# Kernel optimization log

Measured on AMD Instinct MI355X. Metric: run time of the kernel, lower is better.

Reference implementation:

```python
import jax, jax.numpy as jnp
import numpy as np

N_U, N_I, E = 100000, 100000, 600000
F_U, F_I, H, OUT = 96, 160, 128, 64
EPS = 1e-5


def _params(key):
    ks = jax.random.split(key, 20)
    n = lambda i, s: (jax.random.normal(ks[i], s, jnp.float32) * 0.05)
    p = {
        # lazy per-type input projections
        'Wp_u': n(0, (F_U, H)), 'bp_u': jnp.zeros((H,), jnp.float32),
        'Wp_i': n(1, (F_I, H)), 'bp_i': jnp.zeros((H,), jnp.float32),
        # layer 0 SAGE (in=H, out=H): lin_l (neighbors, bias), lin_r (root, no bias)
        'Wl0_ui': n(2, (H, H)), 'bl0_ui': jnp.zeros((H,), jnp.float32), 'Wr0_ui': n(3, (H, H)),
        'Wl0_iu': n(4, (H, H)), 'bl0_iu': jnp.zeros((H,), jnp.float32), 'Wr0_iu': n(5, (H, H)),
        'g0_u': jnp.ones((H,), jnp.float32), 'b0_u': jnp.zeros((H,), jnp.float32),
        'g0_i': jnp.ones((H,), jnp.float32), 'b0_i': jnp.zeros((H,), jnp.float32),
        # layer 1 SAGE (in=H, out=OUT)
        'Wl1_ui': n(6, (H, OUT)), 'bl1_ui': jnp.zeros((OUT,), jnp.float32), 'Wr1_ui': n(7, (H, OUT)),
        'Wl1_iu': n(8, (H, OUT)), 'bl1_iu': jnp.zeros((OUT,), jnp.float32), 'Wr1_iu': n(9, (H, OUT)),
        'g1_u': jnp.ones((OUT,), jnp.float32), 'b1_u': jnp.zeros((OUT,), jnp.float32),
        'g1_i': jnp.ones((OUT,), jnp.float32), 'b1_i': jnp.zeros((OUT,), jnp.float32),
    }
    return p


def setup_inputs() -> dict:
    key = jax.random.key(0)
    k0, k1, k2, k3, kp = jax.random.split(key, 5)
    inp = {
        'x_user': jax.random.normal(k0, (N_U, F_U), jnp.float32),
        'x_item': jax.random.normal(k1, (N_I, F_I), jnp.float32),
        'edge_ui': jax.random.randint(k2, (2, E), 0, N_U),  # row0: src user idx, row1: dst item idx
        'edge_iu': jax.random.randint(k3, (2, E), 0, N_I),  # row0: src item idx, row1: dst user idx
    }
    inp.update(_params(kp))
    return inp


def _seg_mean(x_src, src, dst, n_dst):
    # gather source features [E, C], scatter-mean into destinations [n_dst, C]
    msg = x_src[src]
    s = jax.ops.segment_sum(msg, dst, num_segments=n_dst)
    cnt = jax.ops.segment_sum(jnp.ones((dst.shape[0], 1), x_src.dtype), dst, num_segments=n_dst)
    return s / jnp.maximum(cnt, 1.0)


def _sage(x_src, x_dst, edge, Wl, bl, Wr, n_dst):
    agg = _seg_mean(x_src, edge[0], edge[1], n_dst)
    return agg @ Wl + bl + x_dst @ Wr


def _ln(h, g, b):
    m = jnp.mean(h, axis=-1, keepdims=True)
    v = jnp.mean(jnp.square(h - m), axis=-1, keepdims=True)
    return (h - m) * jax.lax.rsqrt(v + EPS) * g + b


def reference(x_user, x_item, edge_ui, edge_iu,
              Wp_u, bp_u, Wp_i, bp_i,
              Wl0_ui, bl0_ui, Wr0_ui, Wl0_iu, bl0_iu, Wr0_iu,
              g0_u, b0_u, g0_i, b0_i,
              Wl1_ui, bl1_ui, Wr1_ui, Wl1_iu, bl1_iu, Wr1_iu,
              g1_u, b1_u, g1_i, b1_i):
    # per-type input projection + ReLU
    h_u = jax.nn.relu(x_user @ Wp_u + bp_u)
    h_i = jax.nn.relu(x_item @ Wp_i + bp_i)
    # layer 0: HeteroConv(sum) of SAGEConv per edge type, then per-type LN + ReLU (dropout = eval identity)
    h_i1 = _sage(h_u, h_i, edge_ui, Wl0_ui, bl0_ui, Wr0_ui, N_I)
    h_u1 = _sage(h_i, h_u, edge_iu, Wl0_iu, bl0_iu, Wr0_iu, N_U)
    h_u1 = jax.nn.relu(_ln(h_u1, g0_u, b0_u))
    h_i1 = jax.nn.relu(_ln(h_i1, g0_i, b0_i))
    # layer 1 (final): SAGE -> LN, no ReLU/dropout
    h_i2 = _sage(h_u1, h_i1, edge_ui, Wl1_ui, bl1_ui, Wr1_ui, N_I)
    h_u2 = _sage(h_i1, h_u1, edge_iu, Wl1_iu, bl1_iu, Wr1_iu, N_U)
    h_u2 = _ln(h_u2, g1_u, b1_u)
    h_i2 = _ln(h_i2, g1_i, b1_i)
    return h_u2, h_i2
```

## Files before the change

kernel.cpp:

```cpp
#include <hip/hip_runtime.h>

typedef __attribute__((ext_vector_type(8))) __bf16 bf16x8;
typedef __attribute__((ext_vector_type(4))) float floatx4;
typedef __attribute__((ext_vector_type(8))) unsigned short ushort8v;
typedef __attribute__((ext_vector_type(4))) unsigned short ushort4v;

namespace {
constexpr int kNU = 100000, kNI = 100000, kE = 600000;
constexpr int kFU = 96, kFI = 160, kH = 128, kOUT = 64;
constexpr float kEPS = 1e-5f;
constexpr int kM = 32;
constexpr int kNCHUNK = 98;
constexpr int kNBLK = kNU / kM;
constexpr int kEB = (kE + 255) / 256;
constexpr int kPART = kNU / 8;
}

__device__ __forceinline__ unsigned short f2b(float f) {
  unsigned u = __builtin_bit_cast(unsigned, f);
  u += 0x7FFFu + ((u >> 16) & 1u);
  return (unsigned short)(u >> 16);
}
__device__ __forceinline__ float b2f(unsigned short h) {
  return __builtin_bit_cast(float, (unsigned)h << 16);
}
__device__ __forceinline__ void split3(float v, unsigned short& h,
                                       unsigned short& m, unsigned short& l) {
  h = f2b(v);
  const float r1 = v - b2f(h);
  m = f2b(r1);
  const float r2 = r1 - b2f(m);
  l = f2b(r2);
}
__device__ __forceinline__ void split2(float v, unsigned short& h,
                                       unsigned short& m) {
  h = f2b(v);
  m = f2b(v - b2f(h));
}
__device__ __forceinline__ bf16x8 ldb8(const unsigned short* p) {
  return __builtin_bit_cast(bf16x8, *(const ushort8v*)p);
}
__device__ __forceinline__ floatx4 mfma16(bf16x8 a, bf16x8 b, floatx4 c) {
  return __builtin_amdgcn_mfma_f32_16x16x32_bf16(a, b, c, 0, 0, 0);
}
__device__ __forceinline__ unsigned short* ab_ptr(void* base, int plane, int r,
                                                  int bo) {
  return (unsigned short*)((char*)base + plane * 8192 + r * 256 +
                           (bo ^ ((r & 7) << 4)));
}
__device__ __forceinline__ void gload_lds16(const void* g, void* l) {
  __builtin_amdgcn_global_load_lds(
      (const __attribute__((address_space(1))) void*)g,
      (__attribute__((address_space(3))) void*)l, 16, 0, 0);
}
__device__ __forceinline__ void split8(const float4& x, const float4& y,
                                       bf16x8& h8, bf16x8& m8) {
  ushort8v h, m;
  const float* p0 = &x.x;
  const float* p1 = &y.x;
#pragma unroll
  for (int u = 0; u < 4; ++u) {
    unsigned short th, tm;
    split2(p0[u], th, tm);
    h[u] = th; m[u] = tm;
    split2(p1[u], th, tm);
    h[4 + u] = th; m[4 + u] = tm;
  }
  h8 = __builtin_bit_cast(bf16x8, h);
  m8 = __builtin_bit_cast(bf16x8, m);
}

struct WcvtArgs {
  const float* src[10];
  unsigned short* dh[10];
  unsigned short* dm[10];
  unsigned short* dl[10];
  int K[10], N[10];
};
__global__ __launch_bounds__(256) void wcvt(WcvtArgs a) {
  const int m = blockIdx.y;
  const int K = a.K[m], N = a.N[m];
  const int idx = blockIdx.x * 256 + threadIdx.x;
  if (idx < K * N) {
    const int n = idx / K, k = idx - n * K;
    unsigned short h, mm, l;
    split3(a.src[m][(size_t)k * N + n], h, mm, l);
    a.dh[m][idx] = h;
    a.dm[m][idx] = mm;
    a.dl[m][idx] = l;
  }
}

__global__ void zero_int(int* __restrict__ p, int n) {
  int i = blockIdx.x * blockDim.x + threadIdx.x;
  const int st = gridDim.x * blockDim.x;
  for (; i < n; i += st) p[i] = 0;
}

__global__ __launch_bounds__(1024) void scanA(const int* __restrict__ cnt_u,
                                              const int* __restrict__ cnt_i,
                                              int* ptr_u, int* ptr_i, int* tot) {
  __shared__ int sh[1024];
  const int dir = blockIdx.y;
  const int* cnt = dir ? cnt_i : cnt_u;
  int* ptr = dir ? ptr_i : ptr_u;
  const int t = threadIdx.x;
  const int i = blockIdx.x * 1024 + t;
  const int v = (i < kNU) ? cnt[i] : 0;
  sh[t] = v;
  __syncthreads();
  for (int o = 1; o < 1024; o <<= 1) {
    const int y = (t >= o) ? sh[t - o] : 0;
    __syncthreads();
    sh[t] += y;
    __syncthreads();
  }
  if (i < kNU) ptr[i] = sh[t] - v;
  if (t == 1023) tot[dir * 128 + blockIdx.x] = sh[1023];
}

__global__ __launch_bounds__(128) void scanB(int* tot) {
  __shared__ int sh[128];
  int* tp = tot + blockIdx.x * 128;
  const int t = threadIdx.x;
  const int v = (t < kNCHUNK) ? tp[t] : 0;
  sh[t] = v;
  __syncthreads();
  for (int o = 1; o < 128; o <<= 1) {
    const int y = (t >= o) ? sh[t - o] : 0;
    __syncthreads();
    sh[t] += y;
    __syncthreads();
  }
  if (t < kNCHUNK) tp[t] = sh[t] - v;
}

__global__ __launch_bounds__(1024) void scanC(int* ptr_u, int* ptr_i,
                                              const int* __restrict__ tot,
                                              int* cur_u, int* cur_i) {
  const int dir = blockIdx.y;
  int* ptr = dir ? ptr_i : ptr_u;
  int* cur = dir ? cur_i : cur_u;
  const int i = blockIdx.x * 1024 + threadIdx.x;
  if (i < kNU) {
    const int v = ptr[i] + tot[dir * 128 + blockIdx.x];
    ptr[i] = v;
    cur[i] = v;
  }
}

template <int F>
__device__ __forceinline__ void proj_body(
    const float* __restrict__ x, const unsigned short* __restrict__ Wh,
    const unsigned short* __restrict__ Wm, const unsigned short* __restrict__ Wl,
    const float* __restrict__ bias, float* __restrict__ out, int blk,
    unsigned short* sh) {
  constexpr int AS = F + 8, KC = F / 32;
  unsigned short* Ah = sh;
  unsigned short* Am = sh + kM * AS;
  unsigned short* Al = sh + 2 * kM * AS;
  const int tid = threadIdx.x;
  const size_t row0 = (size_t)blk * kM;
  for (int c = tid; c < kM * (F / 4); c += 256) {
    const int r = c / (F / 4), j = c % (F / 4);
    const float4 v = *(const float4*)&x[(row0 + r) * F + j * 4];
    const float* vv = &v.x;
    ushort4v h4, m4, l4;
#pragma unroll
    for (int u = 0; u < 4; ++u) {
      unsigned short th, tm, tl;
      split3(vv[u], th, tm, tl);
      h4[u] = th; m4[u] = tm; l4[u] = tl;
    }
    *(ushort4v*)&Ah[r * AS + j * 4] = h4;
    *(ushort4v*)&Am[r * AS + j * 4] = m4;
    *(ushort4v*)&Al[r * AS + j * 4] = l4;
  }
  const int lane = tid & 63, w = tid >> 6, q = lane >> 4, ln = lane & 15;
  floatx4 acc[2][2] = {}, accL[2][2] = {};
  __syncthreads();
#pragma unroll
  for (int kc = 0; kc < KC; ++kc) {
    bf16x8 bh[2], bm[2], bl_[2];
#pragma unroll
    for (int t = 0; t < 2; ++t) {
      const int off = (w * 32 + t * 16 + ln) * F + kc * 32 + q * 8;
      bh[t] = ldb8(&Wh[off]);
      bm[t] = ldb8(&Wm[off]);
      bl_[t] = ldb8(&Wl[off]);
    }
#pragma unroll
    for (int mt = 0; mt < 2; ++mt) {
      const int ro = mt * 16 + ln, co = kc * 32 + q * 8;
      const bf16x8 ah = ldb8(&Ah[ro * AS + co]);
      const bf16x8 am = ldb8(&Am[ro * AS + co]);
      const bf16x8 al = ldb8(&Al[ro * AS + co]);
#pragma unroll
      for (int t = 0; t < 2; ++t) {
        acc[mt][t] = mfma16(ah, bh[t], acc[mt][t]);
        floatx4 cl = accL[mt][t];
        cl = mfma16(ah, bm[t], cl);
        cl = mfma16(am, bh[t], cl);
        cl = mfma16(ah, bl_[t], cl);
        cl = mfma16(al, bh[t], cl);
        cl = mfma16(am, bm[t], cl);
        accL[mt][t] = cl;
      }
    }
  }
#pragma unroll
  for (int t = 0; t < 2; ++t) {
    const int col = w * 32 + t * 16 + ln;
    const float bv = bias[col];
#pragma unroll
    for (int mt = 0; mt < 2; ++mt)
#pragma unroll
      for (int r = 0; r < 4; ++r)
        out[(row0 + mt * 16 + q * 4 + r) * kH + col] =
            fmaxf((acc[mt][t][r] + accL[mt][t][r]) + bv, 0.f);
  }
}

__global__ __launch_bounds__(256, 4) void hist_proj(
    const int* __restrict__ eui, const int* __restrict__ eiu, int* cnt_i,
    int* cnt_u, const float* __restrict__ x,
    const unsigned short* __restrict__ Wh, const unsigned short* __restrict__ Wm,
    const unsigned short* __restrict__ Wl, const float* __restrict__ bias,
    float* __restrict__ out) {
  __shared__ __align__(16) unsigned short sh[3 * kM * (kFU + 8)];
  if (blockIdx.x < 8 * kEB) {
    const int part = blockIdx.x & 7, slice = blockIdx.x >> 3;
    const int e = slice * 256 + threadIdx.x;
    if (e < kE) {
      const int di = eui[kE + e];
      if (di / kPART == part) atomicAdd(&cnt_i[di], 1);
      const int du = eiu[kE + e];
      if (du / kPART == part) atomicAdd(&cnt_u[du], 1);
    }
  } else {
    proj_body<kFU>(x, Wh, Wm, Wl, bias, out, blockIdx.x - 8 * kEB, sh);
  }
}

__global__ __launch_bounds__(256, 4) void fill_proj(
    const int* __restrict__ eui, const int* __restrict__ eiu, int* cur_i,
    int* cur_u, int* __restrict__ col_ui, int* __restrict__ col_iu,
    const float* __restrict__ x, const unsigned short* __restrict__ Wh,
    const unsigned short* __restrict__ Wm, const unsigned short* __restrict__ Wl,
    const float* __restrict__ bias, float* __restrict__ out) {
  __shared__ __align__(16) unsigned short sh[3 * kM * (kFI + 8)];
  if (blockIdx.x < 8 * kEB) {
    const int part = blockIdx.x & 7, slice = blockIdx.x >> 3;
    const int e = slice * 256 + threadIdx.x;
    if (e < kE) {
      const int di = eui[kE + e];
      if (di / kPART == part) {
        const int p = atomicAdd(&cur_i[di], 1);
        col_ui[p] = eui[e];
      }
      const int du = eiu[kE + e];
      if (du / kPART == part) {
        const int p2 = atomicAdd(&cur_u[du], 1);
        col_iu[p2] = eiu[e];
      }
    }
  } else {
    proj_body<kFI>(x, Wh, Wm, Wl, bias, out, blockIdx.x - 8 * kEB, sh);
  }
}

struct AggArgs {
  const float* src[2];
  const int* ptr[2];
  const int* cur[2];
  const int* col[2];
  float* out[2];
};
template <int W>
__global__ __launch_bounds__(256) void agg2(AggArgs a) {
  const int dir = blockIdx.y;
  const int w = threadIdx.x >> 6, lane = threadIdx.x & 63;
  const int row = blockIdx.x * 4 + w;
  const float* __restrict__ feat = a.src[dir];
  const int* __restrict__ col = a.col[dir];
  const int beg = a.ptr[dir][row], end = a.cur[dir][row];
  const float inv = 1.0f / fmaxf((float)(end - beg), 1.0f);
  if (W == 128) {
    float s0 = 0.f, s1 = 0.f;
    for (int e = beg; e < end; e += 8) {
      const int n = end - e;
      int cidx[8];
#pragma unroll
      for (int j = 0; j < 8; ++j) cidx[j] = col[(j < n) ? (e + j) : e];
      __builtin_amdgcn_sched_barrier(0);
      float2 v[8];
#pragma unroll
      for (int j = 0; j < 8; ++j)
        if (j < n) v[j] = *(const float2*)&feat[(size_t)cidx[j] * 128 + lane * 2];
      __builtin_amdgcn_sched_barrier(0);
#pragma unroll
      for (int j = 0; j < 8; ++j)
        if (j < n) { s0 += v[j].x; s1 += v[j].y; }
    }
    float2 o;
    o.x = s0 * inv;
    o.y = s1 * inv;
    *(float2*)&a.out[dir][(size_t)row * 128 + lane * 2] = o;
  } else {
    float s = 0.f;
    for (int e = beg; e < end; e += 8) {
      const int n = end - e;
      int cidx[8];
#pragma unroll
      for (int j = 0; j < 8; ++j) cidx[j] = col[(j < n) ? (e + j) : e];
      __builtin_amdgcn_sched_barrier(0);
      float v[8];
#pragma unroll
      for (int j = 0; j < 8; ++j)
        if (j < n) v[j] = feat[(size_t)cidx[j] * 64 + lane];
      __builtin_amdgcn_sched_barrier(0);
#pragma unroll
      for (int j = 0; j < 8; ++j)
        if (j < n) s += v[j];
    }
    a.out[dir][(size_t)row * 64 + lane] = s * inv;
  }
}

struct FsArgs {
  const float* agg[2];
  const float* root[2];
  const unsigned short *WLh[2], *WLm[2];
  const unsigned short *WRh[2], *WRm[2];
  const unsigned short *ZBh[2], *ZBm[2];
  const float *bl[2], *g[2], *b[2];
  float* out[2];
  float* zout[2];
};
__global__ __launch_bounds__(256, 4) void sage0(FsArgs a) {
  constexpr int NOUT = 128;
  __shared__ __align__(16) char Lds[32768];
  float* Cs = (float*)Lds;
  const int tid = threadIdx.x;
  const int dir = blockIdx.y;
  const size_t row0 = (size_t)blockIdx.x * kM;
  const float* __restrict__ agg = a.agg[dir];
  const float* __restrict__ root = a.root[dir];
  const unsigned short* __restrict__ WLh = a.WLh[dir];
  const unsigned short* __restrict__ WLm = a.WLm[dir];
  const unsigned short* __restrict__ WRh = a.WRh[dir];
  const unsigned short* __restrict__ WRm = a.WRm[dir];
  const int lane = tid & 63, w = tid >> 6, q = lane >> 4, ln = lane & 15;

  {
    const char* g0 = (const char*)agg + row0 * 512;
    const char* g1 = (const char*)root + row0 * 512;
#pragma unroll
    for (int c = 0; c < 4; ++c) {
      const int sbase = (w * 4 + c) * 1024;
      const int s = sbase + lane * 16;
      const int soff = s ^ (((s >> 9) & 7) << 4);
      gload_lds16(g0 + soff, Lds + sbase);
      gload_lds16(g1 + soff, Lds + 16384 + sbase);
    }
  }

  floatx4 acc[2][2] = {}, accL[2][2] = {};
  __syncthreads();
#pragma unroll
  for (int kc = 0; kc < 4; ++kc) {
    bf16x8 BL[2][2], BR[2][2];
#pragma unroll
    for (int t = 0; t < 2; ++t) {
      const int off = (w * 32 + t * 16 + ln) * kH + kc * 32 + q * 8;
      BL[0][t] = ldb8(&WLh[off]);
      BL[1][t] = ldb8(&WLm[off]);
      BR[0][t] = ldb8(&WRh[off]);
      BR[1][t] = ldb8(&WRm[off]);
    }
#pragma unroll
    for (int mt = 0; mt < 2; ++mt) {
      const int ro = mt * 16 + ln;
      const int lb = ro * 512 + kc * 128 + q * 32;
      const int xr = (ro & 7) << 4;
      const float4 fa0 = *(const float4*)(Lds + (lb ^ xr));
      const float4 fa1 = *(const float4*)(Lds + ((lb + 16) ^ xr));
      const float4 fr0 = *(const float4*)(Lds + 16384 + (lb ^ xr));
      const float4 fr1 = *(const float4*)(Lds + 16384 + ((lb + 16) ^ xr));
      bf16x8 a1h, a1m, a2h, a2m;
      split8(fa0, fa1, a1h, a1m);
      split8(fr0, fr1, a2h, a2m);
#pragma unroll
      for (int t = 0; t < 2; ++t) {
        floatx4 c = acc[mt][t];
        c = mfma16(a1h, BL[0][t], c);
        c = mfma16(a2h, BR[0][t], c);
        acc[mt][t] = c;
        floatx4 cl = accL[mt][t];
        cl = mfma16(a1h, BL[1][t], cl);
        cl = mfma16(a1m, BL[0][t], cl);
        cl = mfma16(a2h, BR[1][t], cl);
        cl = mfma16(a2m, BR[0][t], cl);
        accL[mt][t] = cl;
      }
    }
  }
  __syncthreads();
  const float* __restrict__ blv = a.bl[dir];
#pragma unroll
  for (int t = 0; t < 2; ++t) {
    const int colx = (w * 2 + t) * 16 + ln;
    const float bv = blv[colx];
#pragma unroll
    for (int mt = 0; mt < 2; ++mt)
#pragma unroll
      for (int r = 0; r < 4; ++r)
        Cs[(mt * 16 + q * 4 + r) * (NOUT + 1) + colx] =
            (acc[mt][t][r] + accL[mt][t][r]) + bv;
  }
  __syncthreads();
  const int r = tid >> 3, sub = tid & 7;
  const float* __restrict__ gg = a.g[dir];
  const float* __restrict__ bb = a.b[dir];
  float vals[16], s = 0.f;
#pragma unroll
  for (int j = 0; j < 16; ++j) {
    const float v = Cs[r * (NOUT + 1) + sub * 16 + j];
    vals[j] = v;
    s += v;
  }
#pragma unroll
  for (int o = 1; o < 8; o <<= 1) s += __shfl_xor(s, o, 64);
  const float mean = s * (1.0f / NOUT);
  float s2 = 0.f;
#pragma unroll
  for (int j = 0; j < 16; ++j) {
    const float d = vals[j] - mean;
    s2 += d * d;
  }
#pragma unroll
  for (int o = 1; o < 8; o <<= 1) s2 += __shfl_xor(s2, o, 64);
  const float rstd = rsqrtf(s2 * (1.0f / NOUT) + kEPS);
  float* op = a.out[dir] + (row0 + r) * NOUT + sub * 16;
  float zv[16];
#pragma unroll
  for (int j = 0; j < 16; j += 4) {
    float4 o4;
    float* oo = &o4.x;
#pragma unroll
    for (int jj = 0; jj < 4; ++jj) {
      const float hv = fmaxf((vals[j + jj] - mean) * rstd * gg[sub * 16 + j + jj] +
                                 bb[sub * 16 + j + jj],
                             0.f);
      oo[jj] = hv;
      zv[j + jj] = hv;
    }
    *(float4*)&op[j] = o4;
  }
  __syncthreads();
#pragma unroll
  for (int j = 0; j < 16; j += 8) {
    ushort8v h8, m8;
#pragma unroll
    for (int u = 0; u < 8; ++u) {
      unsigned short th, tm;
      split2(zv[j + u], th, tm);
      h8[u] = th; m8[u] = tm;
    }
    const int bo = sub * 32 + j * 2;
    *(ushort8v*)ab_ptr(Lds, 0, r, bo) = h8;
    *(ushort8v*)ab_ptr(Lds, 1, r, bo) = m8;
  }
  const unsigned short* __restrict__ ZBh = a.ZBh[dir];
  const unsigned short* __restrict__ ZBm = a.ZBm[dir];
  floatx4 zacc[2] = {}, zaccL[2] = {};
  __syncthreads();
#pragma unroll
  for (int kc = 0; kc < 4; ++kc) {
    const int off = (w * 16 + ln) * kH + kc * 32 + q * 8;
    const bf16x8 zbh = ldb8(&ZBh[off]);
    const bf16x8 zbm = ldb8(&ZBm[off]);
#pragma unroll
    for (int mt = 0; mt < 2; ++mt) {
      const int ro = mt * 16 + ln, cob = kc * 64 + q * 16;
      const bf16x8 ah = ldb8(ab_ptr(Lds, 0, ro, cob));
      const bf16x8 am = ldb8(ab_ptr(Lds, 1, ro, cob));
      zacc[mt] = mfma16(ah, zbh, zacc[mt]);
      floatx4 cl = zaccL[mt];
      cl = mfma16(ah, zbm, cl);
      cl = mfma16(am, zbh, cl);
      zaccL[mt] = cl;
    }
  }
  float* __restrict__ zo = a.zout[dir];
  const int zcol = w * 16 + ln;
#pragma unroll
  for (int mt = 0; mt < 2; ++mt)
#pragma unroll
    for (int rr = 0; rr < 4; ++rr)
      zo[(row0 + mt * 16 + q * 4 + rr) * kOUT + zcol] =
          zacc[mt][rr] + zaccL[mt][rr];
}

struct S1Args {
  const float* root[2];
  const float* aggz[2];
  const unsigned short *Bh[2], *Bm[2];
  const float *bl[2], *g[2], *b[2];
  float* out[2];
};
__global__ __launch_bounds__(256, 5) void sage1(S1Args a) {
  constexpr int NOUT = kOUT;
  __shared__ __align__(16) unsigned short Ab[2 * kM * kH];
  float* Cs = (float*)Ab;
  const int tid = threadIdx.x, dir = blockIdx.y;
  const size_t row0 = (size_t)blockIdx.x * kM;
  const float* __restrict__ root = a.root[dir];
  const unsigned short* __restrict__ Bh = a.Bh[dir];
  const unsigned short* __restrict__ Bm = a.Bm[dir];
  const int lane = tid & 63, w = tid >> 6, q = lane >> 4, ln = lane & 15;

  float4 va[4];
#pragma unroll
  for (int k = 0; k < 4; ++k) {
    const int c = tid + k * 256, r = c >> 5, j = c & 31;
    va[k] = *(const float4*)&root[(row0 + r) * kH + j * 4];
  }
  bf16x8 Bh4[4], Bm4[4];
#pragma unroll
  for (int kc = 0; kc < 4; ++kc) {
    const int off = (w * 16 + ln) * kH + kc * 32 + q * 8;
    Bh4[kc] = ldb8(&Bh[off]);
    Bm4[kc] = ldb8(&Bm[off]);
  }
  __builtin_amdgcn_sched_barrier(0);
#pragma unroll
  for (int k = 0; k < 4; ++k) {
    const int c = tid + k * 256, r = c >> 5, j = c & 31;
    const float* vv = &va[k].x;
    ushort4v h4, m4;
#pragma unroll
    for (int u = 0; u < 4; ++u) {
      unsigned short th, tm;
      split2(vv[u], th, tm);
      h4[u] = th; m4[u] = tm;
    }
    *(ushort4v*)ab_ptr(Ab, 0, r, j * 8) = h4;
    *(ushort4v*)ab_ptr(Ab, 1, r, j * 8) = m4;
  }
  floatx4 acc[2] = {}, accL[2] = {};
  __syncthreads();
#pragma unroll
  for (int kc = 0; kc < 4; ++kc) {
#pragma unroll
    for (int mt = 0; mt < 2; ++mt) {
      const int ro = mt * 16 + ln, cob = kc * 64 + q * 16;
      const bf16x8 ah = ldb8(ab_ptr(Ab, 0, ro, cob));
      const bf16x8 am = ldb8(ab_ptr(Ab, 1, ro, cob));
      acc[mt] = mfma16(ah, Bh4[kc], acc[mt]);
      floatx4 cl = accL[mt];
      cl = mfma16(ah, Bm4[kc], cl);
      cl = mfma16(am, Bh4[kc], cl);
      accL[mt] = cl;
    }
  }
  __syncthreads();
  const float* __restrict__ blv = a.bl[dir];
  {
    const int col = w * 16 + ln;
    const float bv = blv[col];
#pragma unroll
    for (int mt = 0; mt < 2; ++mt)
#pragma unroll
      for (int r = 0; r < 4; ++r)
        Cs[(mt * 16 + q * 4 + r) * (NOUT + 1) + col] =
            (acc[mt][r] + accL[mt][r]) + bv;
  }
  __syncthreads();
  const int r = tid >> 3, sub = tid & 7;
  const float* __restrict__ az = a.aggz[dir];
  const float* __restrict__ gg = a.g[dir];
  const float* __restrict__ bb = a.b[dir];
  const float4 az0 = *(const float4*)&az[(row0 + r) * NOUT + sub * 8];
  const float4 az1 = *(const float4*)&az[(row0 + r) * NOUT + sub * 8 + 4];
  float vals[8], s = 0.f;
#pragma unroll
  for (int j = 0; j < 8; ++j) {
    const float v = Cs[r * (NOUT + 1) + sub * 8 + j] +
                    (j < 4 ? (&az0.x)[j] : (&az1.x)[j - 4]);
    vals[j] = v;
    s += v;
  }
#pragma unroll
  for (int o = 1; o < 8; o <<= 1) s += __shfl_xor(s, o, 64);
  const float mean = s * (1.0f / NOUT);
  float s2 = 0.f;
#pragma unroll
  for (int j = 0; j < 8; ++j) {
    const float d = vals[j] - mean;
    s2 += d * d;
  }
#pragma unroll
  for (int o = 1; o < 8; o <<= 1) s2 += __shfl_xor(s2, o, 64);
  const float rstd = rsqrtf(s2 * (1.0f / NOUT) + kEPS);
  float* op = a.out[dir] + (row0 + r) * NOUT + sub * 8;
#pragma unroll
  for (int j = 0; j < 8; j += 4) {
    float4 o4;
    float* oo = &o4.x;
#pragma unroll
    for (int jj = 0; jj < 4; ++jj)
      oo[jj] = (vals[j + jj] - mean) * rstd * gg[sub * 8 + j + jj] +
               bb[sub * 8 + j + jj];
    *(float4*)&op[j] = o4;
  }
}

extern "C" void kernel_launch(void* const* d_in, const int* in_sizes, int n_in,
                              void* d_out, int out_size, void* d_ws, size_t ws_size,
                              hipStream_t stream) {
  (void)in_sizes; (void)n_in; (void)out_size; (void)ws_size;
  const float* x_u    = (const float*)d_in[0];
  const float* x_i    = (const float*)d_in[1];
  const int*   e_ui   = (const int*)d_in[2];
  const int*   e_iu   = (const int*)d_in[3];
  const float* Wp_u   = (const float*)d_in[4];
  const float* bp_u   = (const float*)d_in[5];
  const float* Wp_i   = (const float*)d_in[6];
  const float* bp_i   = (const float*)d_in[7];
  const float* Wl0_ui = (const float*)d_in[8];
  const float* bl0_ui = (const float*)d_in[9];
  const float* Wr0_ui = (const float*)d_in[10];
  const float* Wl0_iu = (const float*)d_in[11];
  const float* bl0_iu = (const float*)d_in[12];
  const float* Wr0_iu = (const float*)d_in[13];
  const float* g0_u   = (const float*)d_in[14];
  const float* b0_u   = (const float*)d_in[15];
  const float* g0_i   = (const float*)d_in[16];
  const float* b0_i   = (const float*)d_in[17];
  const float* Wl1_ui = (const float*)d_in[18];
  const float* bl1_ui = (const float*)d_in[19];
  const float* Wr1_ui = (const float*)d_in[20];
  const float* Wl1_iu = (const float*)d_in[21];
  const float* bl1_iu = (const float*)d_in[22];
  const float* Wr1_iu = (const float*)d_in[23];
  const float* g1_u   = (const float*)d_in[24];
  const float* b1_u   = (const float*)d_in[25];
  const float* g1_i   = (const float*)d_in[26];
  const float* b1_i   = (const float*)d_in[27];

  float* pf = (float*)d_ws;
  const size_t NH = (size_t)kNU * kH;
  float* hu0 = pf;
  float* hi0 = pf + NH;
  float* b2  = pf + 2 * NH;
  float* b3  = pf + 3 * NH;
  float* aggzI = hi0;
  float* aggzU = hi0 + (size_t)kNU * kOUT;
  unsigned short* wh = (unsigned short*)(pf + 4 * NH);
  unsigned short* wm = wh + 131072;
  unsigned short* wl = wm + 131072;
  int* pi = (int*)(wl + 131072);
  int* cnt_u = pi; pi += kNU;
  int* cnt_i = pi; pi += kNU;
  int* ptr_u = pi; pi += kNU;
  int* ptr_i = pi; pi += kNU;
  int* cur_u = pi; pi += kNU;
  int* cur_i = pi; pi += kNU;
  int* tot   = pi; pi += 2 * 128;
  int* col_ui = pi; pi += kE;
  int* col_iu = pi; pi += kE;

  const int oPu = 0, oPi = 12288, o0Lui = 32768, o0Rui = 49152,
            o0Liu = 65536, o0Riu = 81920, o1Lui = 98304, o1Rui = 106496,
            o1Liu = 114688, o1Riu = 122880;

  float* out_u = (float*)d_out;
  float* out_i = out_u + (size_t)kNU * kOUT;
  float* Zu = out_u;
  float* Zi = out_i;

  WcvtArgs wa;
  const float* wsrc[10] = {Wp_u, Wp_i, Wl0_ui, Wr0_ui, Wl0_iu, Wr0_iu,
                           Wl1_ui, Wr1_ui, Wl1_iu, Wr1_iu};
  const int woff[10] = {oPu, oPi, o0Lui, o0Rui, o0Liu, o0Riu,
                        o1Lui, o1Rui, o1Liu, o1Riu};
  const int wK[10] = {kFU, kFI, kH, kH, kH, kH, kH, kH, kH, kH};
  const int wN[10] = {kH, kH, kH, kH, kH, kH, kOUT, kOUT, kOUT, kOUT};
  for (int i = 0; i < 10; ++i) {
    wa.src[i] = wsrc[i];
    wa.dh[i] = wh + woff[i];
    wa.dm[i] = wm + woff[i];
    wa.dl[i] = wl + woff[i];
    wa.K[i] = wK[i];
    wa.N[i] = wN[i];
  }
  wcvt<<<dim3(80, 10), 256, 0, stream>>>(wa);

  zero_int<<<256, 256, 0, stream>>>(cnt_u, 2 * kNU);
  hist_proj<<<8 * kEB + kNBLK, 256, 0, stream>>>(e_ui, e_iu, cnt_i, cnt_u, x_u,
                                                 wh + oPu, wm + oPu, wl + oPu,
                                                 bp_u, hu0);
  scanA<<<dim3(kNCHUNK, 2), 1024, 0, stream>>>(cnt_u, cnt_i, ptr_u, ptr_i, tot);
  scanB<<<2, 128, 0, stream>>>(tot);
  scanC<<<dim3(kNCHUNK, 2), 1024, 0, stream>>>(ptr_u, ptr_i, tot, cur_u, cur_i);
  fill_proj<<<8 * kEB + kNBLK, 256, 0, stream>>>(e_ui, e_iu, cur_i, cur_u,
                                                 col_ui, col_iu, x_i, wh + oPi,
                                                 wm + oPi, wl + oPi, bp_i, hi0);

  AggArgs g0;
  g0.src[0] = hu0; g0.ptr[0] = ptr_i; g0.cur[0] = cur_i; g0.col[0] = col_ui;
  g0.out[0] = b2;
  g0.src[1] = hi0; g0.ptr[1] = ptr_u; g0.cur[1] = cur_u; g0.col[1] = col_iu;
  g0.out[1] = b3;
  agg2<kH><<<dim3(kNU / 4, 2), 256, 0, stream>>>(g0);

  FsArgs a0;
  a0.agg[0] = b2; a0.root[0] = hi0;
  a0.WLh[0] = wh + o0Lui; a0.WLm[0] = wm + o0Lui;
  a0.WRh[0] = wh + o0Rui; a0.WRm[0] = wm + o0Rui;
  a0.ZBh[0] = wh + o1Liu; a0.ZBm[0] = wm + o1Liu;
  a0.bl[0] = bl0_ui; a0.g[0] = g0_i; a0.b[0] = b0_i;
  a0.out[0] = b2;
  a0.zout[0] = Zi;
  a0.agg[1] = b3; a0.root[1] = hu0;
  a0.WLh[1] = wh + o0Liu; a0.WLm[1] = wm + o0Liu;
  a0.WRh[1] = wh + o0Riu; a0.WRm[1] = wm + o0Riu;
  a0.ZBh[1] = wh + o1Lui; a0.ZBm[1] = wm + o1Lui;
  a0.bl[1] = bl0_iu; a0.g[1] = g0_u; a0.b[1] = b0_u;
  a0.out[1] = b3;
  a0.zout[1] = Zu;
  sage0<<<dim3(kNBLK, 2), 256, 0, stream>>>(a0);

  AggArgs g1;
  g1.src[0] = Zu; g1.ptr[0] = ptr_i; g1.cur[0] = cur_i; g1.col[0] = col_ui;
  g1.out[0] = aggzI;
  g1.src[1] = Zi; g1.ptr[1] = ptr_u; g1.cur[1] = cur_u; g1.col[1] = col_iu;
  g1.out[1] = aggzU;
  agg2<kOUT><<<dim3(kNU / 4, 2), 256, 0, stream>>>(g1);

  S1Args s1;
  s1.root[0] = b2; s1.aggz[0] = aggzI;
  s1.Bh[0] = wh + o1Rui; s1.Bm[0] = wm + o1Rui;
  s1.bl[0] = bl1_ui; s1.g[0] = g1_i; s1.b[0] = b1_i; s1.out[0] = out_i;
  s1.root[1] = b3; s1.aggz[1] = aggzU;
  s1.Bh[1] = wh + o1Riu; s1.Bm[1] = wm + o1Riu;
  s1.bl[1] = bl1_iu; s1.g[1] = g1_u; s1.b[1] = b1_u; s1.out[1] = out_u;
  sage1<<<dim3(kNBLK, 2), 256, 0, stream>>>(s1);
}
```

Measured before the change: 713.3 us.

## Store intermediate features as pre-split swizzled bf16 hi/lo planes

```diff
diff --git a/kernel.cpp b/kernel.cpp
--- a/kernel.cpp
+++ b/kernel.cpp
@@ -37,7 +37,7 @@
   h = f2b(v);
   m = f2b(v - b2f(h));
 }
-__device__ __forceinline__ bf16x8 ldb8(const unsigned short* p) {
+__device__ __forceinline__ bf16x8 ldb8(const void* p) {
   return __builtin_bit_cast(bf16x8, *(const ushort8v*)p);
 }
 __device__ __forceinline__ floatx4 mfma16(bf16x8 a, bf16x8 b, floatx4 c) {
@@ -53,22 +53,7 @@
       (const __attribute__((address_space(1))) void*)g,
       (__attribute__((address_space(3))) void*)l, 16, 0, 0);
 }
-__device__ __forceinline__ void split8(const float4& x, const float4& y,
-                                       bf16x8& h8, bf16x8& m8) {
-  ushort8v h, m;
-  const float* p0 = &x.x;
-  const float* p1 = &y.x;
-#pragma unroll
-  for (int u = 0; u < 4; ++u) {
-    unsigned short th, tm;
-    split2(p0[u], th, tm);
-    h[u] = th; m[u] = tm;
-    split2(p1[u], th, tm);
-    h[4 + u] = th; m[4 + u] = tm;
-  }
-  h8 = __builtin_bit_cast(bf16x8, h);
-  m8 = __builtin_bit_cast(bf16x8, m);
-}
+
 
 struct WcvtArgs {
   const float* src[10];
@@ -153,7 +138,7 @@
 __device__ __forceinline__ void proj_body(
     const float* __restrict__ x, const unsigned short* __restrict__ Wh,
     const unsigned short* __restrict__ Wm, const unsigned short* __restrict__ Wl,
-    const float* __restrict__ bias, float* __restrict__ out, int blk,
+    const float* __restrict__ bias, unsigned short* __restrict__ out, int blk,
     unsigned short* sh) {
   constexpr int AS = F + 8, KC = F / 32;
   unsigned short* Ah = sh;
@@ -215,9 +200,16 @@
 #pragma unroll
     for (int mt = 0; mt < 2; ++mt)
 #pragma unroll
-      for (int r = 0; r < 4; ++r)
-        out[(row0 + mt * 16 + q * 4 + r) * kH + col] =
-            fmaxf((acc[mt][t][r] + accL[mt][t][r]) + bv, 0.f);
+      for (int r = 0; r < 4; ++r) {
+        const int rl = mt * 16 + q * 4 + r;
+        const float val = fmaxf((acc[mt][t][r] + accL[mt][t][r]) + bv, 0.f);
+        unsigned short hh, mm;
+        split2(val, hh, mm);
+        char* rowp = (char*)out + (row0 + rl) * 512;
+        const int bo = (col * 2) ^ ((rl & 7) << 4);
+        *(unsigned short*)(rowp + bo) = hh;
+        *(unsigned short*)(rowp + 256 + bo) = mm;
+      }
   }
 }
 
@@ -226,7 +218,7 @@
     int* cnt_u, const float* __restrict__ x,
     const unsigned short* __restrict__ Wh, const unsigned short* __restrict__ Wm,
     const unsigned short* __restrict__ Wl, const float* __restrict__ bias,
-    float* __restrict__ out) {
+    unsigned short* __restrict__ out) {
   __shared__ __align__(16) unsigned short sh[3 * kM * (kFU + 8)];
   if (blockIdx.x < 8 * kEB) {
     const int part = blockIdx.x & 7, slice = blockIdx.x >> 3;
@@ -247,7 +239,7 @@
     int* cur_u, int* __restrict__ col_ui, int* __restrict__ col_iu,
     const float* __restrict__ x, const unsigned short* __restrict__ Wh,
     const unsigned short* __restrict__ Wm, const unsigned short* __restrict__ Wl,
-    const float* __restrict__ bias, float* __restrict__ out) {
+    const float* __restrict__ bias, unsigned short* __restrict__ out) {
   __shared__ __align__(16) unsigned short sh[3 * kM * (kFI + 8)];
   if (blockIdx.x < 8 * kEB) {
     const int part = blockIdx.x & 7, slice = blockIdx.x >> 3;
@@ -270,22 +262,22 @@
 }
 
 struct AggArgs {
-  const float* src[2];
+  const void* src[2];
   const int* ptr[2];
   const int* cur[2];
   const int* col[2];
-  float* out[2];
+  void* out[2];
 };
 template <int W>
 __global__ __launch_bounds__(256) void agg2(AggArgs a) {
   const int dir = blockIdx.y;
   const int w = threadIdx.x >> 6, lane = threadIdx.x & 63;
   const int row = blockIdx.x * 4 + w;
-  const float* __restrict__ feat = a.src[dir];
   const int* __restrict__ col = a.col[dir];
   const int beg = a.ptr[dir][row], end = a.cur[dir][row];
   const float inv = 1.0f / fmaxf((float)(end - beg), 1.0f);
   if (W == 128) {
+    const char* __restrict__ Tb = (const char*)a.src[dir];
     float s0 = 0.f, s1 = 0.f;
     for (int e = beg; e < end; e += 8) {
       const int n = end - e;
@@ -293,20 +285,35 @@
 #pragma unroll
       for (int j = 0; j < 8; ++j) cidx[j] = col[(j < n) ? (e + j) : e];
       __builtin_amdgcn_sched_barrier(0);
-      float2 v[8];
+      unsigned hm0[8], hm1[8];
 #pragma unroll
       for (int j = 0; j < 8; ++j)
-        if (j < n) v[j] = *(const float2*)&feat[(size_t)cidx[j] * 128 + lane * 2];
+        if (j < n) {
+          const char* rp = Tb + (size_t)cidx[j] * 512;
+          const int bo = (lane * 4) ^ ((cidx[j] & 7) << 4);
+          hm0[j] = *(const unsigned*)(rp + bo);
+          hm1[j] = *(const unsigned*)(rp + 256 + bo);
+        }
       __builtin_amdgcn_sched_barrier(0);
 #pragma unroll
       for (int j = 0; j < 8; ++j)
-        if (j < n) { s0 += v[j].x; s1 += v[j].y; }
-    }
-    float2 o;
-    o.x = s0 * inv;
-    o.y = s1 * inv;
-    *(float2*)&a.out[dir][(size_t)row * 128 + lane * 2] = o;
+        if (j < n) {
+          s0 += b2f((unsigned short)hm0[j]) + b2f((unsigned short)hm1[j]);
+          s1 += b2f((unsigned short)(hm0[j] >> 16)) +
+                b2f((unsigned short)(hm1[j] >> 16));
+        }
+    }
+    s0 *= inv;
+    s1 *= inv;
+    unsigned short h0, m0, h1, m1;
+    split2(s0, h0, m0);
+    split2(s1, h1, m1);
+    char* op = (char*)a.out[dir] + (size_t)row * 512;
+    const int bo = (lane * 4) ^ ((row & 7) << 4);
+    *(unsigned*)(op + bo) = (unsigned)h0 | ((unsigned)h1 << 16);
+    *(unsigned*)(op + 256 + bo) = (unsigned)m0 | ((unsigned)m1 << 16);
   } else {
+    const float* __restrict__ feat = (const float*)a.src[dir];
     float s = 0.f;
     for (int e = beg; e < end; e += 8) {
       const int n = end - e;
@@ -323,29 +330,38 @@
       for (int j = 0; j < 8; ++j)
         if (j < n) s += v[j];
     }
-    a.out[dir][(size_t)row * 64 + lane] = s * inv;
+    ((float*)a.out[dir])[(size_t)row * 64 + lane] = s * inv;
   }
 }
 
 struct FsArgs {
-  const float* agg[2];
-  const float* root[2];
+  const unsigned short* agg[2];
+  const unsigned short* root[2];
   const unsigned short *WLh[2], *WLm[2];
   const unsigned short *WRh[2], *WRm[2];
   const unsigned short *ZBh[2], *ZBm[2];
   const float *bl[2], *g[2], *b[2];
-  float* out[2];
+  unsigned short* out[2];
   float* zout[2];
 };
-__global__ __launch_bounds__(256, 4) void sage0(FsArgs a) {
+
+#define LOADW_S0(B, KC)                                                  \
+  {                                                                      \
+    const int o0_ = (w * 32 + 0 * 16 + ln) * kH + (KC) * 32 + q * 8;     \
+    const int o1_ = (w * 32 + 1 * 16 + ln) * kH + (KC) * 32 + q * 8;     \
+    BLh[B][0] = ldb8(&WLh[o0_]); BLh[B][1] = ldb8(&WLh[o1_]);            \
+    BLm[B][0] = ldb8(&WLm[o0_]); BLm[B][1] = ldb8(&WLm[o1_]);            \
+    BRh[B][0] = ldb8(&WRh[o0_]); BRh[B][1] = ldb8(&WRh[o1_]);            \
+    BRm[B][0] = ldb8(&WRm[o0_]); BRm[B][1] = ldb8(&WRm[o1_]);            \
+  }
+
+__global__ __launch_bounds__(256, 5) void sage0(FsArgs a) {
   constexpr int NOUT = 128;
   __shared__ __align__(16) char Lds[32768];
   float* Cs = (float*)Lds;
   const int tid = threadIdx.x;
   const int dir = blockIdx.y;
   const size_t row0 = (size_t)blockIdx.x * kM;
-  const float* __restrict__ agg = a.agg[dir];
-  const float* __restrict__ root = a.root[dir];
   const unsigned short* __restrict__ WLh = a.WLh[dir];
   const unsigned short* __restrict__ WLm = a.WLm[dir];
   const unsigned short* __restrict__ WRh = a.WRh[dir];
@@ -353,54 +369,45 @@
   const int lane = tid & 63, w = tid >> 6, q = lane >> 4, ln = lane & 15;
 
   {
-    const char* g0 = (const char*)agg + row0 * 512;
-    const char* g1 = (const char*)root + row0 * 512;
+    const char* g0 = (const char*)a.agg[dir] + row0 * 512;
+    const char* g1 = (const char*)a.root[dir] + row0 * 512;
 #pragma unroll
     for (int c = 0; c < 4; ++c) {
       const int sbase = (w * 4 + c) * 1024;
-      const int s = sbase + lane * 16;
-      const int soff = s ^ (((s >> 9) & 7) << 4);
-      gload_lds16(g0 + soff, Lds + sbase);
-      gload_lds16(g1 + soff, Lds + 16384 + sbase);
-    }
-  }
-
+      gload_lds16(g0 + sbase + lane * 16, Lds + sbase);
+      gload_lds16(g1 + sbase + lane * 16, Lds + 16384 + sbase);
+    }
+  }
+  bf16x8 BLh[2][2], BLm[2][2], BRh[2][2], BRm[2][2];
+  LOADW_S0(0, 0);
   floatx4 acc[2][2] = {}, accL[2][2] = {};
   __syncthreads();
 #pragma unroll
   for (int kc = 0; kc < 4; ++kc) {
-    bf16x8 BL[2][2], BR[2][2];
-#pragma unroll
-    for (int t = 0; t < 2; ++t) {
-      const int off = (w * 32 + t * 16 + ln) * kH + kc * 32 + q * 8;
-      BL[0][t] = ldb8(&WLh[off]);
-      BL[1][t] = ldb8(&WLm[off]);
-      BR[0][t] = ldb8(&WRh[off]);
-      BR[1][t] = ldb8(&WRm[off]);
-    }
+    if (kc < 3) LOADW_S0((kc + 1) & 1, kc + 1);
+    __builtin_amdgcn_sched_barrier(0);
 #pragma unroll
     for (int mt = 0; mt < 2; ++mt) {
       const int ro = mt * 16 + ln;
-      const int lb = ro * 512 + kc * 128 + q * 32;
       const int xr = (ro & 7) << 4;
-      const float4 fa0 = *(const float4*)(Lds + (lb ^ xr));
-      const float4 fa1 = *(const float4*)(Lds + ((lb + 16) ^ xr));
-      const float4 fr0 = *(const float4*)(Lds + 16384 + (lb ^ xr));
-      const float4 fr1 = *(const float4*)(Lds + 16384 + ((lb + 16) ^ xr));
-      bf16x8 a1h, a1m, a2h, a2m;
-      split8(fa0, fa1, a1h, a1m);
-      split8(fr0, fr1, a2h, a2m);
+      const int hb = (kc * 64 + q * 16) ^ xr;
+      const char* r1 = Lds + ro * 512;
+      const char* r2 = Lds + 16384 + ro * 512;
+      const bf16x8 a1h = ldb8(r1 + hb);
+      const bf16x8 a1m = ldb8(r1 + 256 + hb);
+      const bf16x8 a2h = ldb8(r2 + hb);
+      const bf16x8 a2m = ldb8(r2 + 256 + hb);
 #pragma unroll
       for (int t = 0; t < 2; ++t) {
         floatx4 c = acc[mt][t];
-        c = mfma16(a1h, BL[0][t], c);
-        c = mfma16(a2h, BR[0][t], c);
+        c = mfma16(a1h, BLh[kc & 1][t], c);
+        c = mfma16(a2h, BRh[kc & 1][t], c);
         acc[mt][t] = c;
         floatx4 cl = accL[mt][t];
-        cl = mfma16(a1h, BL[1][t], cl);
-        cl = mfma16(a1m, BL[0][t], cl);
-        cl = mfma16(a2h, BR[1][t], cl);
-        cl = mfma16(a2m, BR[0][t], cl);
+        cl = mfma16(a1h, BLm[kc & 1][t], cl);
+        cl = mfma16(a1m, BLh[kc & 1][t], cl);
+        cl = mfma16(a2h, BRm[kc & 1][t], cl);
+        cl = mfma16(a2m, BRh[kc & 1][t], cl);
         accL[mt][t] = cl;
       }
     }
@@ -441,36 +448,38 @@
 #pragma unroll
   for (int o = 1; o < 8; o <<= 1) s2 += __shfl_xor(s2, o, 64);
   const float rstd = rsqrtf(s2 * (1.0f / NOUT) + kEPS);
-  float* op = a.out[dir] + (row0 + r) * NOUT + sub * 16;
   float zv[16];
-#pragma unroll
-  for (int j = 0; j < 16; j += 4) {
-    float4 o4;
-    float* oo = &o4.x;
-#pragma unroll
-    for (int jj = 0; jj < 4; ++jj) {
-      const float hv = fmaxf((vals[j + jj] - mean) * rstd * gg[sub * 16 + j + jj] +
-                                 bb[sub * 16 + j + jj],
-                             0.f);
-      oo[jj] = hv;
-      zv[j + jj] = hv;
-    }
-    *(float4*)&op[j] = o4;
-  }
-  __syncthreads();
-#pragma unroll
-  for (int j = 0; j < 16; j += 8) {
-    ushort8v h8, m8;
-#pragma unroll
-    for (int u = 0; u < 8; ++u) {
+  ushort8v h8[2], m8[2];
+#pragma unroll
+  for (int hf = 0; hf < 2; ++hf)
+#pragma unroll
+    for (int j = 0; j < 8; ++j) {
+      const int jj = hf * 8 + j;
+      const float hv = fmaxf(
+          (vals[jj] - mean) * rstd * gg[sub * 16 + jj] + bb[sub * 16 + jj], 0.f);
+      zv[jj] = hv;
       unsigned short th, tm;
-      split2(zv[j + u], th, tm);
-      h8[u] = th; m8[u] = tm;
-    }
-    const int bo = sub * 32 + j * 2;
-    *(ushort8v*)ab_ptr(Lds, 0, r, bo) = h8;
-    *(ushort8v*)ab_ptr(Lds, 1, r, bo) = m8;
-  }
+      split2(hv, th, tm);
+      h8[hf][j] = th;
+      m8[hf][j] = tm;
+    }
+  {
+    char* hp = (char*)a.out[dir] + (row0 + r) * 512;
+    const int xr = (r & 7) << 4;
+#pragma unroll
+    for (int hf = 0; hf < 2; ++hf) {
+      const int bo = (sub * 32 + hf * 16) ^ xr;
+      *(ushort8v*)(hp + bo) = h8[hf];
+      *(ushort8v*)(hp + 256 + bo) = m8[hf];
+    }
+  }
+  __syncthreads();
+#pragma unroll
+  for (int hf = 0; hf < 2; ++hf) {
+    *(ushort8v*)ab_ptr(Lds, 0, r, sub * 32 + hf * 16) = h8[hf];
+    *(ushort8v*)ab_ptr(Lds, 1, r, sub * 32 + hf * 16) = m8[hf];
+  }
+  (void)zv;
   const unsigned short* __restrict__ ZBh = a.ZBh[dir];
   const unsigned short* __restrict__ ZBm = a.ZBm[dir];
   floatx4 zacc[2] = {}, zaccL[2] = {};
@@ -503,28 +512,29 @@
 }
 
 struct S1Args {
-  const float* root[2];
+  const unsigned short* root[2];
   const float* aggz[2];
   const unsigned short *Bh[2], *Bm[2];
   const float *bl[2], *g[2], *b[2];
   float* out[2];
 };
-__global__ __launch_bounds__(256, 5) void sage1(S1Args a) {
+__global__ __launch_bounds__(256, 6) void sage1(S1Args a) {
   constexpr int NOUT = kOUT;
-  __shared__ __align__(16) unsigned short Ab[2 * kM * kH];
-  float* Cs = (float*)Ab;
+  __shared__ __align__(16) char Lds[16384];
+  float* Cs = (float*)Lds;
   const int tid = threadIdx.x, dir = blockIdx.y;
   const size_t row0 = (size_t)blockIdx.x * kM;
-  const float* __restrict__ root = a.root[dir];
   const unsigned short* __restrict__ Bh = a.Bh[dir];
   const unsigned short* __restrict__ Bm = a.Bm[dir];
   const int lane = tid & 63, w = tid >> 6, q = lane >> 4, ln = lane & 15;
 
-  float4 va[4];
-#pragma unroll
-  for (int k = 0; k < 4; ++k) {
-    const int c = tid + k * 256, r = c >> 5, j = c & 31;
-    va[k] = *(const float4*)&root[(row0 + r) * kH + j * 4];
+  {
+    const char* g0 = (const char*)a.root[dir] + row0 * 512;
+#pragma unroll
+    for (int c = 0; c < 4; ++c) {
+      const int sbase = (w * 4 + c) * 1024;
+      gload_lds16(g0 + sbase + lane * 16, Lds + sbase);
+    }
   }
   bf16x8 Bh4[4], Bm4[4];
 #pragma unroll
@@ -533,30 +543,18 @@
     Bh4[kc] = ldb8(&Bh[off]);
     Bm4[kc] = ldb8(&Bm[off]);
   }
-  __builtin_amdgcn_sched_barrier(0);
-#pragma unroll
-  for (int k = 0; k < 4; ++k) {
-    const int c = tid + k * 256, r = c >> 5, j = c & 31;
-    const float* vv = &va[k].x;
-    ushort4v h4, m4;
-#pragma unroll
-    for (int u = 0; u < 4; ++u) {
-      unsigned short th, tm;
-      split2(vv[u], th, tm);
-      h4[u] = th; m4[u] = tm;
-    }
-    *(ushort4v*)ab_ptr(Ab, 0, r, j * 8) = h4;
-    *(ushort4v*)ab_ptr(Ab, 1, r, j * 8) = m4;
-  }
   floatx4 acc[2] = {}, accL[2] = {};
   __syncthreads();
 #pragma unroll
   for (int kc = 0; kc < 4; ++kc) {
 #pragma unroll
     for (int mt = 0; mt < 2; ++mt) {
-      const int ro = mt * 16 + ln, cob = kc * 64 + q * 16;
-      const bf16x8 ah = ldb8(ab_ptr(Ab, 0, ro, cob));
-      const bf16x8 am = ldb8(ab_ptr(Ab, 1, ro, cob));
+      const int ro = mt * 16 + ln;
+      const int xr = (ro & 7) << 4;
+      const int hb = (kc * 64 + q * 16) ^ xr;
+      const char* rp = Lds + ro * 512;
+      const bf16x8 ah = ldb8(rp + hb);
+      const bf16x8 am = ldb8(rp + 256 + hb);
       acc[mt] = mfma16(ah, Bh4[kc], acc[mt]);
       floatx4 cl = accL[mt];
       cl = mfma16(ah, Bm4[kc], cl);
@@ -651,12 +649,12 @@
 
   float* pf = (float*)d_ws;
   const size_t NH = (size_t)kNU * kH;
-  float* hu0 = pf;
-  float* hi0 = pf + NH;
-  float* b2  = pf + 2 * NH;
-  float* b3  = pf + 3 * NH;
-  float* aggzI = hi0;
-  float* aggzU = hi0 + (size_t)kNU * kOUT;
+  unsigned short* Thu0 = (unsigned short*)pf;
+  unsigned short* Thi0 = (unsigned short*)(pf + NH);
+  unsigned short* TaggI = (unsigned short*)(pf + 2 * NH);
+  unsigned short* TaggU = (unsigned short*)(pf + 3 * NH);
+  float* aggzI = pf + NH;
+  float* aggzU = pf + NH + (size_t)kNU * kOUT;
   unsigned short* wh = (unsigned short*)(pf + 4 * NH);
   unsigned short* wm = wh + 131072;
   unsigned short* wl = wm + 131072;
@@ -700,35 +698,35 @@
   zero_int<<<256, 256, 0, stream>>>(cnt_u, 2 * kNU);
   hist_proj<<<8 * kEB + kNBLK, 256, 0, stream>>>(e_ui, e_iu, cnt_i, cnt_u, x_u,
                                                  wh + oPu, wm + oPu, wl + oPu,
-                                                 bp_u, hu0);
+                                                 bp_u, Thu0);
   scanA<<<dim3(kNCHUNK, 2), 1024, 0, stream>>>(cnt_u, cnt_i, ptr_u, ptr_i, tot);
   scanB<<<2, 128, 0, stream>>>(tot);
   scanC<<<dim3(kNCHUNK, 2), 1024, 0, stream>>>(ptr_u, ptr_i, tot, cur_u, cur_i);
   fill_proj<<<8 * kEB + kNBLK, 256, 0, stream>>>(e_ui, e_iu, cur_i, cur_u,
                                                  col_ui, col_iu, x_i, wh + oPi,
-                                                 wm + oPi, wl + oPi, bp_i, hi0);
+                                                 wm + oPi, wl + oPi, bp_i, Thi0);
 
   AggArgs g0;
-  g0.src[0] = hu0; g0.ptr[0] = ptr_i; g0.cur[0] = cur_i; g0.col[0] = col_ui;
-  g0.out[0] = b2;
-  g0.src[1] = hi0; g0.ptr[1] = ptr_u; g0.cur[1] = cur_u; g0.col[1] = col_iu;
-  g0.out[1] = b3;
+  g0.src[0] = Thu0; g0.ptr[0] = ptr_i; g0.cur[0] = cur_i; g0.col[0] = col_ui;
+  g0.out[0] = TaggI;
+  g0.src[1] = Thi0; g0.ptr[1] = ptr_u; g0.cur[1] = cur_u; g0.col[1] = col_iu;
+  g0.out[1] = TaggU;
   agg2<kH><<<dim3(kNU / 4, 2), 256, 0, stream>>>(g0);
 
   FsArgs a0;
-  a0.agg[0] = b2; a0.root[0] = hi0;
+  a0.agg[0] = TaggI; a0.root[0] = Thi0;
   a0.WLh[0] = wh + o0Lui; a0.WLm[0] = wm + o0Lui;
   a0.WRh[0] = wh + o0Rui; a0.WRm[0] = wm + o0Rui;
   a0.ZBh[0] = wh + o1Liu; a0.ZBm[0] = wm + o1Liu;
   a0.bl[0] = bl0_ui; a0.g[0] = g0_i; a0.b[0] = b0_i;
-  a0.out[0] = b2;
+  a0.out[0] = TaggI;
   a0.zout[0] = Zi;
-  a0.agg[1] = b3; a0.root[1] = hu0;
+  a0.agg[1] = TaggU; a0.root[1] = Thu0;
   a0.WLh[1] = wh + o0Liu; a0.WLm[1] = wm + o0Liu;
   a0.WRh[1] = wh + o0Riu; a0.WRm[1] = wm + o0Riu;
   a0.ZBh[1] = wh + o1Lui; a0.ZBm[1] = wm + o1Lui;
   a0.bl[1] = bl0_iu; a0.g[1] = g0_u; a0.b[1] = b0_u;
-  a0.out[1] = b3;
+  a0.out[1] = TaggU;
   a0.zout[1] = Zu;
   sage0<<<dim3(kNBLK, 2), 256, 0, stream>>>(a0);
 
@@ -740,10 +738,10 @@
   agg2<kOUT><<<dim3(kNU / 4, 2), 256, 0, stream>>>(g1);
 
   S1Args s1;
-  s1.root[0] = b2; s1.aggz[0] = aggzI;
+  s1.root[0] = TaggI; s1.aggz[0] = aggzI;
   s1.Bh[0] = wh + o1Rui; s1.Bm[0] = wm + o1Rui;
   s1.bl[0] = bl1_ui; s1.g[0] = g1_i; s1.b[0] = b1_i; s1.out[0] = out_i;
-  s1.root[1] = b3; s1.aggz[1] = aggzU;
+  s1.root[1] = TaggU; s1.aggz[1] = aggzU;
   s1.Bh[1] = wh + o1Riu; s1.Bm[1] = wm + o1Riu;
   s1.bl[1] = bl1_iu; s1.g[1] = g1_u; s1.b[1] = b1_u; s1.out[1] = out_u;
   sage1<<<dim3(kNBLK, 2), 256, 0, stream>>>(s1);
```

After: 863.3 us. 21.0% more time.
